# Kernel optimization log

Hardware: AMD Instinct MI355X
Metric: run time of the kernel (lower is better)

Reference implementation:

```python
import jax, jax.numpy as jnp
import numpy as np

# positions 0,1 = input tensor dims; positions 2,3 = output tensor dims (single entity type)

def _set_partitions(elems):
    if not elems:
        yield []
        return
    first, rest = elems[0], elems[1:]
    for p in _set_partitions(rest):
        for i in range(len(p)):
            yield p[:i] + [p[i] + [first]] + p[i + 1:]
    # note: generator above already covers merging; add singleton case

def _all_set_partitions(elems):
    if not elems:
        return [[]]
    first, rest = elems[0], elems[1:]
    out = []
    for p in _all_set_partitions(rest):
        for i in range(len(p)):
            out.append(p[:i] + [p[i] + [first]] + p[i + 1:])
        out.append([[first]] + p)
    return out

PARTITIONS = _all_set_partitions([0, 1, 2, 3])  # Bell(4) = 15 equivariant partitions


def _apply_partition(X, part, eye, ones):
    """Dense equivalent of diag -> pool -> broadcast -> undiag -> reindex for one partition.
    X: [b, c, n, n]. Returns [b, c, n, n]."""
    pos2blk = {p: bi for bi, blk in enumerate(part) for p in blk}
    blk_letter = {bi: 'defg'[bi] for bi in range(len(part))}
    # step 1: diag (repeated letters) + pool (letters dropped from output)
    in_sub = 'bc' + blk_letter[pos2blk[0]] + blk_letter[pos2blk[1]]
    keep = [bi for bi, blk in enumerate(part)
            if any(p < 2 for p in blk) and any(p >= 2 for p in blk)]
    z_sub = 'bc' + ''.join(blk_letter[bi] for bi in keep)
    Z = jnp.einsum(f'{in_sub}->{z_sub}', X)
    # step 2: broadcast + diag-embed into output positions via eye/ones factors
    out_letter = {2: 'p', 3: 'q'}
    operands, subs = [Z], [z_sub]
    for bi, blk in enumerate(part):
        outpos = [p for p in blk if p >= 2]
        if not outpos:
            continue
        if any(p < 2 for p in blk):  # block tied to a surviving input dim
            for p in outpos:
                operands.append(eye)
                subs.append(blk_letter[bi] + out_letter[p])
        else:  # pure broadcast block
            first = outpos[0]
            operands.append(ones)
            subs.append(out_letter[first])
            for p in outpos[1:]:
                operands.append(eye)
                subs.append(out_letter[first] + out_letter[p])
    return jnp.einsum(','.join(subs) + '->bcpq', *operands)


def setup_inputs() -> dict:
    key = jax.random.key(0)
    k1, k2 = jax.random.split(key)
    B, C_IN, C_OUT, N = 4, 96, 96, 256
    stdv = 0.1 / np.sqrt(C_IN)
    X_in = jax.random.normal(k1, (B, C_IN, N, N), dtype=jnp.float32)
    Y_in = jnp.zeros((B, C_IN, N, N), dtype=jnp.float32)  # only provides output shape
    weights = jax.random.uniform(k2, (15, C_IN, C_OUT), minval=-stdv, maxval=stdv, dtype=jnp.float32)
    bias = jnp.ones((1,), dtype=jnp.float32)
    return {'X_in': X_in, 'Y_in': Y_in, 'weights': weights, 'bias': bias}


def reference(X_in, Y_in, weights, bias):
    n = X_in.shape[-1]
    eye = jnp.eye(n, dtype=X_in.dtype)
    ones = jnp.ones((n,), dtype=X_in.dtype)
    Y = None
    for i, part in enumerate(PARTITIONS):
        Yp = _apply_partition(X_in, part, eye, ones)          # [b, c_in, n, n]
        Yp = jnp.einsum('bcpq,co->bopq', Yp, weights[i])       # channel linear
        Y = Yp if Y is None else Y + Yp
    return Y + bias[0]
```

## Files before the change

kernel.cpp:

```cpp
#include <hip/hip_runtime.h>
#include <hip/hip_bf16.h>

#define NN 256
#define CIN 96
#define COUT 96
#define BB 4

typedef __attribute__((ext_vector_type(8))) short short8;
typedef __attribute__((ext_vector_type(4))) float f32x4;

__device__ __forceinline__ float waveReduceSum(float v) {
    #pragma unroll
    for (int m = 32; m >= 1; m >>= 1) v += __shfl_xor(v, m, 64);
    return v;
}

__device__ __forceinline__ unsigned int packbf2(float lo, float hi) {
    __hip_bfloat162 h = __float22bfloat162_rn(make_float2(lo, hi));
    unsigned int u;
    __builtin_memcpy(&u, &h, 4);
    return u;
}

__device__ __forceinline__ short8 u4_to_s8(uint4 u) {
    short8 r;
    __builtin_memcpy(&r, &u, 16);
    return r;
}

__global__ __launch_bounds__(256) void k_aux(const float* __restrict__ X,
                                             float* __restrict__ rows,
                                             float* __restrict__ cols,
                                             float* __restrict__ diag,
                                             float* __restrict__ TSa) {
    const int bc = blockIdx.x;
    const float* Xp = X + (size_t)bc * NN * NN;
    const int tid = threadIdx.x;
    const int wave = tid >> 6, lane = tid & 63;

    __shared__ float rowsL[NN];
    __shared__ float colPart[4][NN];
    __shared__ float sred[8];

    float4 csum = make_float4(0.f, 0.f, 0.f, 0.f);
    for (int p = wave; p < NN; p += 4) {
        float4 v = *(const float4*)(Xp + (size_t)p * NN + lane * 4);
        csum.x += v.x; csum.y += v.y; csum.z += v.z; csum.w += v.w;
        float rs = waveReduceSum(v.x + v.y + v.z + v.w);
        if (lane == 0) rowsL[p] = rs;
    }
    *(float4*)(&colPart[wave][lane * 4]) = csum;
    __syncthreads();

    float col = colPart[0][tid] + colPart[1][tid] + colPart[2][tid] + colPart[3][tid];
    const size_t gb = (size_t)bc * NN;
    cols[gb + tid] = col;
    float rsv = rowsL[tid];
    rows[gb + tid] = rsv;
    float d = Xp[(size_t)tid * (NN + 1)];
    diag[gb + tid] = d;

    float t1 = waveReduceSum(d);
    float s1 = waveReduceSum(rsv);
    if (lane == 0) { sred[wave] = t1; sred[4 + wave] = s1; }
    __syncthreads();
    if (tid == 0) {
        TSa[bc * 2 + 0] = sred[0] + sred[1] + sred[2] + sred[3];
        TSa[bc * 2 + 1] = sred[4] + sred[5] + sred[6] + sred[7];
    }
}

__global__ __launch_bounds__(512) void k_pqg(const float* __restrict__ W,
                                             const float* __restrict__ rows,
                                             const float* __restrict__ cols,
                                             const float* __restrict__ diag,
                                             const float* __restrict__ TSa,
                                             const float* __restrict__ bias,
                                             float* __restrict__ Pw,
                                             float* __restrict__ Qw,
                                             float* __restrict__ Gw) {
    const int bo = blockIdx.x;
    const int b = bo / COUT, o = bo % COUT;
    const int half = threadIdx.x >> 8;
    const int p = threadIdx.x & 255;

    __shared__ float red[5][256];

    float P = 0.f, Q = 0.f, G = 0.f, s = 0.f, gs = 0.f;
    const int cbeg = half * 48, cend = cbeg + 48;
    for (int c = cbeg; c < cend; ++c) {
        const size_t base = (size_t)(b * CIN + c) * NN;
        float r  = rows[base + p];
        float cl = cols[base + p];
        float dg = diag[base + p];
        const float* wp = W + c * COUT + o;
        #define WI(i) wp[(i) * CIN * COUT]
        P += WI(12) * r + WI(7)  * cl + WI(5) * dg;
        Q += WI(13) * r + WI(10) * cl + WI(9) * dg;
        G += WI(3)  * r + WI(1)  * cl + WI(0) * dg;
        float Tv = TSa[(b * CIN + c) * 2 + 0];
        float Sv = TSa[(b * CIN + c) * 2 + 1];
        s  += WI(11) * Tv + WI(14) * Sv;
        gs += WI(2)  * Tv + WI(4)  * Sv;
        #undef WI
    }
    if (half == 1) {
        red[0][p] = P; red[1][p] = Q; red[2][p] = G; red[3][p] = s; red[4][p] = gs;
    }
    __syncthreads();
    if (half == 0) {
        P += red[0][p]; Q += red[1][p]; G += red[2][p]; s += red[3][p]; gs += red[4][p];
        const size_t ob = (size_t)bo * NN;
        Pw[ob + p] = P + s + bias[0];
        Qw[ob + p] = Q;
        Gw[ob + p] = G + gs;
    }
}

#define XPLANE 324
#define WPLANE 100

__global__ __launch_bounds__(512, 1) void k_main(const float* __restrict__ X,
                                                 const float* __restrict__ W,
                                                 const float* __restrict__ Pw,
                                                 const float* __restrict__ Qw,
                                                 const float* __restrict__ Gw,
                                                 float* __restrict__ Y) {
    __shared__ __align__(16) unsigned int XAs[16 * XPLANE];
    __shared__ __align__(16) unsigned int XBs[16 * XPLANE];
    __shared__ __align__(16) unsigned int W8s[16 * WPLANE];
    __shared__ __align__(16) unsigned int W6s[16 * WPLANE];

    const int orig = blockIdx.x + 16 * (blockIdx.y + 16 * blockIdx.z);
    const int work = (orig & 7) * 128 + (orig >> 3);
    const int tq = work & 15, tp = (work >> 4) & 15, b = work >> 8;

    const int tid = threadIdx.x;
    const int w = tid >> 6, lane = tid & 63;
    const int sp = lane >> 2, sq4 = (lane & 3) * 4;
    const int col = lane & 15, g = lane >> 4;

    f32x4 acc[6][2];
    #pragma unroll
    for (int m = 0; m < 6; ++m) {
        acc[m][0] = f32x4{0.f, 0.f, 0.f, 0.f};
        acc[m][1] = f32x4{0.f, 0.f, 0.f, 0.f};
    }

    const float* Xb  = X + (size_t)b * CIN * NN * NN;
    const float* G1  = Xb + (size_t)(tp * 16) * NN + tq * 16;
    const float* G2  = Xb + (size_t)(tq * 16) * NN + tp * 16;
    const float* w8g = W + 8 * CIN * COUT;
    const float* w6g = W + 6 * CIN * COUT;

    for (int c0 = 0; c0 < CIN; c0 += 32) {
        __syncthreads();

        #pragma unroll
        for (int h = 0; h < 2; ++h) {
            const int cw = w + 8 * h;
            const size_t cb = (size_t)(c0 + 2 * cw) * (NN * NN);
            const float* pa = G1 + cb + sp * NN + sq4;
            float4 a0 = *(const float4*)pa;
            float4 a1 = *(const float4*)(pa + NN * NN);
            uint4 pk;
            pk.x = packbf2(a0.x, a1.x);
            pk.y = packbf2(a0.y, a1.y);
            pk.z = packbf2(a0.z, a1.z);
            pk.w = packbf2(a0.w, a1.w);
            *(uint4*)&XAs[cw * XPLANE + sp * 20 + sq4] = pk;

            const float* pb = G2 + cb + sp * NN + sq4;
            float4 b0 = *(const float4*)pb;
            float4 b1 = *(const float4*)(pb + NN * NN);
            unsigned int* dB = &XBs[cw * XPLANE + sp];
            dB[(sq4 + 0) * 20] = packbf2(b0.x, b1.x);
            dB[(sq4 + 1) * 20] = packbf2(b0.y, b1.y);
            dB[(sq4 + 2) * 20] = packbf2(b0.z, b1.z);
            dB[(sq4 + 3) * 20] = packbf2(b0.w, b1.w);
        }
        #pragma unroll
        for (int it = 0; it < 3; ++it) {
            const int i  = tid + it * 512;
            const int cw = i / 96, o = i - cw * 96;
            const int cg = (c0 + 2 * cw) * COUT + o;
            W8s[cw * WPLANE + o] = packbf2(w8g[cg], w8g[cg + COUT]);
            W6s[cw * WPLANE + o] = packbf2(w6g[cg], w6g[cg + COUT]);
        }
        __syncthreads();

        const unsigned int* xab = &XAs[4 * g * XPLANE + w * 20 + col];
        const unsigned int* xbb = &XBs[4 * g * XPLANE + w * 20 + col];
        uint4 u;
        u.x = xab[0]; u.y = xab[XPLANE]; u.z = xab[2 * XPLANE]; u.w = xab[3 * XPLANE];
        short8 xd0 = u4_to_s8(u);
        u.x = xab[160]; u.y = xab[XPLANE + 160]; u.z = xab[2 * XPLANE + 160]; u.w = xab[3 * XPLANE + 160];
        short8 xd1 = u4_to_s8(u);
        u.x = xbb[0]; u.y = xbb[XPLANE]; u.z = xbb[2 * XPLANE]; u.w = xbb[3 * XPLANE];
        short8 xt0 = u4_to_s8(u);
        u.x = xbb[160]; u.y = xbb[XPLANE + 160]; u.z = xbb[2 * XPLANE + 160]; u.w = xbb[3 * XPLANE + 160];
        short8 xt1 = u4_to_s8(u);

        #pragma unroll
        for (int m = 0; m < 6; ++m) {
            const unsigned int* wp8 = &W8s[4 * g * WPLANE + m * 16 + col];
            const unsigned int* wp6 = &W6s[4 * g * WPLANE + m * 16 + col];
            uint4 v8, v6;
            v8.x = wp8[0]; v8.y = wp8[WPLANE]; v8.z = wp8[2 * WPLANE]; v8.w = wp8[3 * WPLANE];
            v6.x = wp6[0]; v6.y = wp6[WPLANE]; v6.z = wp6[2 * WPLANE]; v6.w = wp6[3 * WPLANE];
            short8 w8f = u4_to_s8(v8);
            short8 w6f = u4_to_s8(v6);
            acc[m][0] = __builtin_amdgcn_mfma_f32_16x16x32_bf16(xd0, w8f, acc[m][0], 0, 0, 0);
            acc[m][0] = __builtin_amdgcn_mfma_f32_16x16x32_bf16(xt0, w6f, acc[m][0], 0, 0, 0);
            acc[m][1] = __builtin_amdgcn_mfma_f32_16x16x32_bf16(xd1, w8f, acc[m][1], 0, 0, 0);
            acc[m][1] = __builtin_amdgcn_mfma_f32_16x16x32_bf16(xt1, w6f, acc[m][1], 0, 0, 0);
        }
    }

    const int p0 = tp * 16 + w;
    const int q4 = tq * 16 + g * 4;
    const bool diagblk = (tp == tq);
    #pragma unroll
    for (int m = 0; m < 6; ++m) {
        const int o = m * 16 + col;
        const size_t ob = (size_t)(b * COUT + o) * NN;
        const float4 qf = *(const float4*)&Qw[ob + q4];
        #pragma unroll
        for (int rr = 0; rr < 2; ++rr) {
            const int p = p0 + rr * 8;
            const float pv = Pw[ob + p];
            float4 out;
            out.x = acc[m][rr][0] + pv + qf.x;
            out.y = acc[m][rr][1] + pv + qf.y;
            out.z = acc[m][rr][2] + pv + qf.z;
            out.w = acc[m][rr][3] + pv + qf.w;
            if (diagblk) {
                const float gv = Gw[ob + p];
                const int d = (p & 15) - g * 4;
                if (d == 0) out.x += gv;
                else if (d == 1) out.y += gv;
                else if (d == 2) out.z += gv;
                else if (d == 3) out.w += gv;
            }
            *(float4*)&Y[(ob + p) * NN + q4] = out;
        }
    }
}

extern "C" void kernel_launch(void* const* d_in, const int* in_sizes, int n_in,
                              void* d_out, int out_size, void* d_ws, size_t ws_size,
                              hipStream_t stream) {
    const float* X    = (const float*)d_in[0];
    const float* W    = (const float*)d_in[2];
    const float* bias = (const float*)d_in[3];
    float* Y = (float*)d_out;

    float* ws   = (float*)d_ws;
    const size_t SEG = (size_t)BB * CIN * NN;
    float* rows = ws;
    float* cols = ws + SEG;
    float* diag = ws + 2 * SEG;
    float* Pw   = ws + 3 * SEG;
    float* Qw   = ws + 4 * SEG;
    float* Gw   = ws + 5 * SEG;
    float* TSa  = ws + 6 * SEG;

    k_aux<<<BB * CIN, 256, 0, stream>>>(X, rows, cols, diag, TSa);
    k_pqg<<<BB * COUT, 512, 0, stream>>>(W, rows, cols, diag, TSa, bias, Pw, Qw, Gw);
    k_main<<<dim3(16, 16, BB), 512, 0, stream>>>(X, W, Pw, Qw, Gw, Y);
}
```

Before: 124.0 us.

## Split row-sum reduction across four blocks per plane with partial column sums

```diff
diff --git a/kernel.cpp b/kernel.cpp
--- a/kernel.cpp
+++ b/kernel.cpp
@@ -5,6 +5,8 @@
 #define CIN 96
 #define COUT 96
 #define BB 4
+#define NBC (BB * CIN)
+#define SEG (NBC * NN)
 
 typedef __attribute__((ext_vector_type(8))) short short8;
 typedef __attribute__((ext_vector_type(4))) float f32x4;
@@ -30,86 +32,103 @@
 
 __global__ __launch_bounds__(256) void k_aux(const float* __restrict__ X,
                                              float* __restrict__ rows,
-                                             float* __restrict__ cols,
                                              float* __restrict__ diag,
-                                             float* __restrict__ TSa) {
-    const int bc = blockIdx.x;
-    const float* Xp = X + (size_t)bc * NN * NN;
+                                             float* __restrict__ colsP,
+                                             float* __restrict__ TSp) {
+    const int blk = blockIdx.x;
+    const int ch = blk & 3, bc = blk >> 2;
+    const float* Xp = X + (size_t)bc * (NN * NN) + (size_t)ch * 64 * NN;
     const int tid = threadIdx.x;
-    const int wave = tid >> 6, lane = tid & 63;
-
-    __shared__ float rowsL[NN];
+    const int w = tid >> 6, lane = tid & 63;
+
     __shared__ float colPart[4][NN];
-    __shared__ float sred[8];
+    __shared__ float sred[4];
 
     float4 csum = make_float4(0.f, 0.f, 0.f, 0.f);
-    for (int p = wave; p < NN; p += 4) {
-        float4 v = *(const float4*)(Xp + (size_t)p * NN + lane * 4);
-        csum.x += v.x; csum.y += v.y; csum.z += v.z; csum.w += v.w;
-        float rs = waveReduceSum(v.x + v.y + v.z + v.w);
-        if (lane == 0) rowsL[p] = rs;
-    }
-    *(float4*)(&colPart[wave][lane * 4]) = csum;
+    #pragma unroll
+    for (int b2 = 0; b2 < 2; ++b2) {
+        float4 v[8];
+        #pragma unroll
+        for (int j = 0; j < 8; ++j) {
+            const int r = w * 16 + b2 * 8 + j;
+            v[j] = *(const float4*)(Xp + (size_t)r * NN + lane * 4);
+        }
+        #pragma unroll
+        for (int j = 0; j < 8; ++j) {
+            csum.x += v[j].x; csum.y += v[j].y; csum.z += v[j].z; csum.w += v[j].w;
+            float rs = waveReduceSum(v[j].x + v[j].y + v[j].z + v[j].w);
+            if (lane == 0)
+                rows[(size_t)bc * NN + ch * 64 + w * 16 + b2 * 8 + j] = rs;
+        }
+    }
+    *(float4*)&colPart[w][lane * 4] = csum;
+
+    if (w == 0) {
+        float dv = Xp[(size_t)lane * NN + ch * 64 + lane];
+        diag[(size_t)bc * NN + ch * 64 + lane] = dv;
+        float t1 = waveReduceSum(dv);
+        if (lane == 0) TSp[(ch * NBC + bc) * 2 + 0] = t1;
+    }
     __syncthreads();
 
     float col = colPart[0][tid] + colPart[1][tid] + colPart[2][tid] + colPart[3][tid];
-    const size_t gb = (size_t)bc * NN;
-    cols[gb + tid] = col;
-    float rsv = rowsL[tid];
-    rows[gb + tid] = rsv;
-    float d = Xp[(size_t)tid * (NN + 1)];
-    diag[gb + tid] = d;
-
-    float t1 = waveReduceSum(d);
-    float s1 = waveReduceSum(rsv);
-    if (lane == 0) { sred[wave] = t1; sred[4 + wave] = s1; }
+    colsP[(size_t)ch * SEG + (size_t)bc * NN + tid] = col;
+    float s1 = waveReduceSum(col);
+    if (lane == 0) sred[w] = s1;
     __syncthreads();
-    if (tid == 0) {
-        TSa[bc * 2 + 0] = sred[0] + sred[1] + sred[2] + sred[3];
-        TSa[bc * 2 + 1] = sred[4] + sred[5] + sred[6] + sred[7];
-    }
-}
-
-__global__ __launch_bounds__(512) void k_pqg(const float* __restrict__ W,
-                                             const float* __restrict__ rows,
-                                             const float* __restrict__ cols,
-                                             const float* __restrict__ diag,
-                                             const float* __restrict__ TSa,
-                                             const float* __restrict__ bias,
-                                             float* __restrict__ Pw,
-                                             float* __restrict__ Qw,
-                                             float* __restrict__ Gw) {
+    if (tid == 0)
+        TSp[(ch * NBC + bc) * 2 + 1] = sred[0] + sred[1] + sred[2] + sred[3];
+}
+
+__global__ __launch_bounds__(1024) void k_pqg(const float* __restrict__ W,
+                                              const float* __restrict__ rows,
+                                              const float* __restrict__ diag,
+                                              const float* __restrict__ colsP,
+                                              const float* __restrict__ TSp,
+                                              const float* __restrict__ bias,
+                                              float* __restrict__ Pw,
+                                              float* __restrict__ Qw,
+                                              float* __restrict__ Gw) {
     const int bo = blockIdx.x;
     const int b = bo / COUT, o = bo % COUT;
-    const int half = threadIdx.x >> 8;
+    const int qtr = threadIdx.x >> 8;
     const int p = threadIdx.x & 255;
 
-    __shared__ float red[5][256];
+    __shared__ float red[3][5][256];
 
     float P = 0.f, Q = 0.f, G = 0.f, s = 0.f, gs = 0.f;
-    const int cbeg = half * 48, cend = cbeg + 48;
+    const int cbeg = qtr * 24, cend = cbeg + 24;
     for (int c = cbeg; c < cend; ++c) {
-        const size_t base = (size_t)(b * CIN + c) * NN;
+        const int bcq = b * CIN + c;
+        const size_t base = (size_t)bcq * NN;
         float r  = rows[base + p];
-        float cl = cols[base + p];
+        float cl = colsP[0 * SEG + base + p] + colsP[1 * SEG + base + p]
+                 + colsP[2 * SEG + base + p] + colsP[3 * SEG + base + p];
         float dg = diag[base + p];
         const float* wp = W + c * COUT + o;
         #define WI(i) wp[(i) * CIN * COUT]
         P += WI(12) * r + WI(7)  * cl + WI(5) * dg;
         Q += WI(13) * r + WI(10) * cl + WI(9) * dg;
         G += WI(3)  * r + WI(1)  * cl + WI(0) * dg;
-        float Tv = TSa[(b * CIN + c) * 2 + 0];
-        float Sv = TSa[(b * CIN + c) * 2 + 1];
+        float Tv = TSp[(0 * NBC + bcq) * 2] + TSp[(1 * NBC + bcq) * 2]
+                 + TSp[(2 * NBC + bcq) * 2] + TSp[(3 * NBC + bcq) * 2];
+        float Sv = TSp[(0 * NBC + bcq) * 2 + 1] + TSp[(1 * NBC + bcq) * 2 + 1]
+                 + TSp[(2 * NBC + bcq) * 2 + 1] + TSp[(3 * NBC + bcq) * 2 + 1];
         s  += WI(11) * Tv + WI(14) * Sv;
         gs += WI(2)  * Tv + WI(4)  * Sv;
         #undef WI
     }
-    if (half == 1) {
-        red[0][p] = P; red[1][p] = Q; red[2][p] = G; red[3][p] = s; red[4][p] = gs;
+    if (qtr) {
+        red[qtr - 1][0][p] = P; red[qtr - 1][1][p] = Q; red[qtr - 1][2][p] = G;
+        red[qtr - 1][3][p] = s; red[qtr - 1][4][p] = gs;
     }
     __syncthreads();
-    if (half == 0) {
-        P += red[0][p]; Q += red[1][p]; G += red[2][p]; s += red[3][p]; gs += red[4][p];
+    if (qtr == 0) {
+        P += red[0][0][p] + red[1][0][p] + red[2][0][p];
+        Q += red[0][1][p] + red[1][1][p] + red[2][1][p];
+        G += red[0][2][p] + red[1][2][p] + red[2][2][p];
+        s += red[0][3][p] + red[1][3][p] + red[2][3][p];
+        gs += red[0][4][p] + red[1][4][p] + red[2][4][p];
         const size_t ob = (size_t)bo * NN;
         Pw[ob + p] = P + s + bias[0];
         Qw[ob + p] = Q;
@@ -255,17 +274,16 @@
     const float* bias = (const float*)d_in[3];
     float* Y = (float*)d_out;
 
-    float* ws   = (float*)d_ws;
-    const size_t SEG = (size_t)BB * CIN * NN;
-    float* rows = ws;
-    float* cols = ws + SEG;
-    float* diag = ws + 2 * SEG;
-    float* Pw   = ws + 3 * SEG;
-    float* Qw   = ws + 4 * SEG;
-    float* Gw   = ws + 5 * SEG;
-    float* TSa  = ws + 6 * SEG;
-
-    k_aux<<<BB * CIN, 256, 0, stream>>>(X, rows, cols, diag, TSa);
-    k_pqg<<<BB * COUT, 512, 0, stream>>>(W, rows, cols, diag, TSa, bias, Pw, Qw, Gw);
+    float* ws    = (float*)d_ws;
+    float* rows  = ws;
+    float* diag  = ws + SEG;
+    float* colsP = ws + 2 * (size_t)SEG;
+    float* Pw    = ws + 6 * (size_t)SEG;
+    float* Qw    = ws + 7 * (size_t)SEG;
+    float* Gw    = ws + 8 * (size_t)SEG;
+    float* TSp   = ws + 9 * (size_t)SEG;
+
+    k_aux<<<NBC * 4, 256, 0, stream>>>(X, rows, diag, colsP, TSp);
+    k_pqg<<<BB * COUT, 1024, 0, stream>>>(W, rows, diag, colsP, TSp, bias, Pw, Qw, Gw);
     k_main<<<dim3(16, 16, BB), 512, 0, stream>>>(X, W, Pw, Qw, Gw, Y);
 }
```

Result: slower. 127.8 us (+3.0%).
